# Performance work log

Hardware: AMD Instinct MI355X
Metric: run time of the kernel (lower is better)

## Reference

```python
import jax, jax.numpy as jnp
import numpy as np

D_MODEL = 1024
NUM_HEADS = 16
DEPTH = D_MODEL // NUM_HEADS
B, S = 8, 1024


def setup_inputs() -> dict:
    key = jax.random.key(0)
    ks = jax.random.split(key, 12)
    sc = 0.02
    return {
        "v": jax.random.normal(ks[0], (B, S, D_MODEL), jnp.float32),
        "k": jax.random.normal(ks[1], (B, S, D_MODEL), jnp.float32),
        "q_in": jax.random.normal(ks[2], (B, S, D_MODEL), jnp.float32),
        "mask": jnp.zeros((B, 1, 1, S), jnp.float32),
        "wq_w": jax.random.normal(ks[3], (D_MODEL, D_MODEL), jnp.float32) * sc,
        "wq_b": jnp.zeros((D_MODEL,), jnp.float32),
        "wk_w": jax.random.normal(ks[4], (D_MODEL, D_MODEL), jnp.float32) * sc,
        "wk_b": jnp.zeros((D_MODEL,), jnp.float32),
        "wv_w": jax.random.normal(ks[5], (D_MODEL, D_MODEL), jnp.float32) * sc,
        "wv_b": jnp.zeros((D_MODEL,), jnp.float32),
        "wo_w": jax.random.normal(ks[6], (2 * D_MODEL, D_MODEL), jnp.float32) * sc,
        "wo_b": jnp.zeros((D_MODEL,), jnp.float32),
    }


def _split_heads(x):
    # (B, S, D) -> (B, H, S, depth)
    b, s, _ = x.shape
    return x.reshape(b, s, NUM_HEADS, DEPTH).transpose(0, 2, 1, 3)


def reference(v, k, q_in, mask, wq_w, wq_b, wk_w, wk_b, wv_w, wv_b, wo_w, wo_b):
    q = _split_heads(q_in @ wq_w + wq_b)   # (B,H,Sq,depth)
    kk = _split_heads(k @ wk_w + wk_b)     # (B,H,Sk,depth)
    vv = _split_heads(v @ wv_w + wv_b)     # (B,H,Sk,depth)

    scale = 1.0 / jnp.sqrt(jnp.float32(DEPTH))
    logits = jnp.einsum("bhqd,bhkd->bhqk", q, kk) * scale
    logits = logits + mask * (-1e9)
    attn = jax.nn.softmax(logits, axis=-1)  # dropout inactive (inference)
    ctx = jnp.einsum("bhqk,bhkd->bhqd", attn, vv)

    # (B,H,Sq,depth) -> (B,Sq,D)
    ctx = ctx.transpose(0, 2, 1, 3).reshape(q_in.shape[0], -1, D_MODEL)
    concat = jnp.concatenate([q_in, ctx], axis=-1)  # (B,Sq,2D)
    out = concat @ wo_w + wo_b
    return out
```

## Files before the change

### kernel.cpp

```cpp
#include <hip/hip_runtime.h>

#define NHEADS 16
#define DEPTH  64
#define BATCH  8
#define SEQ    1024
#define DMODEL 1024
#define MTOT   (BATCH*SEQ)

typedef float f32x4 __attribute__((ext_vector_type(4)));
typedef int   i32x4 __attribute__((ext_vector_type(4)));
typedef unsigned short u16;

static __device__ inline u16 f2bf(float x) {
    unsigned int u = __builtin_bit_cast(unsigned int, x);
    u += 0x7FFFu + ((u >> 16) & 1u);
    return (u16)(u >> 16);
}

static __device__ inline unsigned cvt_pk_bf16(float lo, float hi) {
    unsigned r;
    asm("v_cvt_pk_bf16_f32 %0, %1, %2" : "=v"(r) : "v"(lo), "v"(hi));
    return r;
}

static __device__ inline void mfma_bf16(f32x4& acc, i32x4 a, i32x4 b) {
    asm("v_mfma_f32_16x16x32_bf16 %0, %1, %2, %0" : "+v"(acc) : "v"(a), "v"(b));
}

static __device__ inline void gload16(const u16* g, u16* l) {
    __builtin_amdgcn_global_load_lds(
        (const __attribute__((address_space(1))) void*)g,
        (__attribute__((address_space(3))) void*)l,
        16, 0, 0);
}

__global__ __launch_bounds__(256) void cvt_kernel(
    const float* __restrict__ A, const float* __restrict__ B, const float* __restrict__ C,
    u16* __restrict__ Ao, u16* __restrict__ Bo, u16* __restrict__ Co)
{
    const float* src = (blockIdx.y == 0) ? A : (blockIdx.y == 1) ? B : C;
    u16* dst         = (blockIdx.y == 0) ? Ao : (blockIdx.y == 1) ? Bo : Co;
    int i = (blockIdx.x * 256 + threadIdx.x) * 8;
    float4 f0 = *reinterpret_cast<const float4*>(src + i);
    float4 f1 = *reinterpret_cast<const float4*>(src + i + 4);
    uint4 u;
    u.x = cvt_pk_bf16(f0.x, f0.y);
    u.y = cvt_pk_bf16(f0.z, f0.w);
    u.z = cvt_pk_bf16(f1.x, f1.y);
    u.w = cvt_pk_bf16(f1.z, f1.w);
    *reinterpret_cast<uint4*>(dst + i) = u;
}

__global__ __launch_bounds__(256) void transpose_cvt_kernel(
    const float* __restrict__ W, u16* __restrict__ Wt, int K, int N)
{
    __shared__ u16 tile[32][33];
    int n0 = blockIdx.x * 32, k0 = blockIdx.y * 32;
    int tx = threadIdx.x & 31, ty = threadIdx.x >> 5;
    #pragma unroll
    for (int r = 0; r < 32; r += 8)
        tile[r + ty][tx] = f2bf(W[(k0 + r + ty) * N + n0 + tx]);
    __syncthreads();
    #pragma unroll
    for (int r = 0; r < 32; r += 8)
        Wt[(n0 + r + ty) * K + k0 + tx] = tile[tx][r + ty];
}

__global__ __launch_bounds__(256) void proj_kernel(
    const u16* __restrict__ Xq, const u16* __restrict__ Xk, const u16* __restrict__ Xv,
    const u16* __restrict__ Wtq, const u16* __restrict__ Wtk, const u16* __restrict__ Wtv,
    const float* __restrict__ Bq, const float* __restrict__ Bk, const float* __restrict__ Bv,
    u16* __restrict__ Qh, u16* __restrict__ Kh, u16* __restrict__ Vt)
{
    const int z = blockIdx.z;
    const u16* X    = (z == 0) ? Xq  : (z == 1) ? Xk  : Xv;
    const u16* Wt   = (z == 0) ? Wtq : (z == 1) ? Wtk : Wtv;
    const float* Bi = (z == 0) ? Bq  : (z == 1) ? Bk  : Bv;
    u16* Out        = (z == 0) ? Qh  : (z == 1) ? Kh  : Vt;

    __shared__ u16 As[128 * 64];
    __shared__ u16 Bs[128 * 64];

    const int t = threadIdx.x;
    const int m0 = blockIdx.x * 128, n0 = blockIdx.y * 128;
    const int lane = t & 63, w = t >> 6;
    const int wu = __builtin_amdgcn_readfirstlane(w);
    const int wm = w >> 1, wn = w & 1;
    const int lr = lane & 15, lg = lane >> 4;
    const int srow = lane >> 3;
    const int scol = ((lane & 7) ^ (srow & 7)) * 8;

    const u16* ga = X  + (m0 + wu * 32 + srow) * DMODEL + scol;
    const u16* gb = Wt + (n0 + wu * 32 + srow) * DMODEL + scol;
    u16* la = As + wu * 32 * 64;
    u16* lb = Bs + wu * 32 * 64;

    f32x4 acc[4][4];
    #pragma unroll
    for (int i = 0; i < 4; ++i)
        #pragma unroll
        for (int j = 0; j < 4; ++j) acc[i][j] = f32x4{0.f, 0.f, 0.f, 0.f};

    for (int k0 = 0; k0 < DMODEL; k0 += 64) {
        __syncthreads();
        gload16(ga + k0,               la);
        gload16(ga + k0 +  8 * DMODEL, la +  8 * 64);
        gload16(ga + k0 + 16 * DMODEL, la + 16 * 64);
        gload16(ga + k0 + 24 * DMODEL, la + 24 * 64);
        gload16(gb + k0,               lb);
        gload16(gb + k0 +  8 * DMODEL, lb +  8 * 64);
        gload16(gb + k0 + 16 * DMODEL, lb + 16 * 64);
        gload16(gb + k0 + 24 * DMODEL, lb + 24 * 64);
        __syncthreads();
        #pragma unroll
        for (int kk = 0; kk < 2; ++kk) {
            const int pslot = ((kk * 4 + lg) ^ (lr & 7)) << 3;
            i32x4 af[4], bfr[4];
            #pragma unroll
            for (int mi = 0; mi < 4; ++mi)
                af[mi] = *reinterpret_cast<const i32x4*>(
                    &As[(wm * 64 + mi * 16 + lr) * 64 + pslot]);
            #pragma unroll
            for (int ni = 0; ni < 4; ++ni)
                bfr[ni] = *reinterpret_cast<const i32x4*>(
                    &Bs[(wn * 64 + ni * 16 + lr) * 64 + pslot]);
            #pragma unroll
            for (int mi = 0; mi < 4; ++mi)
                #pragma unroll
                for (int ni = 0; ni < 4; ++ni)
                    mfma_bf16(acc[mi][ni], af[mi], bfr[ni]);
        }
    }
    asm volatile("s_nop 7\n\ts_nop 7");
    #pragma unroll
    for (int mi = 0; mi < 4; ++mi)
        #pragma unroll
        for (int ni = 0; ni < 4; ++ni) {
            int n = n0 + wn * 64 + ni * 16 + lr;
            float bv = Bi[n];
            int h = n >> 6, d = n & 63;
            int mb = m0 + wm * 64 + mi * 16 + lg * 4;
            int b = mb >> 10, srw = mb & 1023;
            if (z == 2) {
                uint2 u;
                u.x = cvt_pk_bf16(acc[mi][ni][0] + bv, acc[mi][ni][1] + bv);
                u.y = cvt_pk_bf16(acc[mi][ni][2] + bv, acc[mi][ni][3] + bv);
                *reinterpret_cast<uint2*>(&Vt[(((b << 4) + h) * DEPTH + d) * SEQ + srw]) = u;
            } else if (z == 0) {
                #pragma unroll
                for (int r = 0; r < 4; ++r)
                    Out[(((b << 4) + h) * SEQ + srw + r) * DEPTH + d] = f2bf((acc[mi][ni][r] + bv) * 0.18033688f);
            } else {
                #pragma unroll
                for (int r = 0; r < 4; ++r)
                    Out[(((b << 4) + h) * SEQ + srw + r) * DEPTH + d] = f2bf(acc[mi][ni][r] + bv);
            }
        }
}

__global__ __launch_bounds__(256) void attn_kernel(
    const u16* __restrict__ Qh, const u16* __restrict__ Kh, const u16* __restrict__ Vt,
    const float* __restrict__ mask, u16* __restrict__ CTX)
{
    __shared__ u16 Ks[64 * 64];
    __shared__ u16 Vts[64 * 64];
    __shared__ u16 Ps[4][32 * 64];
    __shared__ float Ms[SEQ];

    const int t = threadIdx.x;
    const int lane = t & 63, w = t >> 6;
    const int lr = lane & 15, lg = lane >> 4;
    const int bh = blockIdx.y;
    const int b = bh >> 4, h = bh & 15;
    const int qw = blockIdx.x * 128 + w * 32;

    const u16* Qp = Qh + bh * (SEQ * DEPTH);
    const u16* Kp = Kh + bh * (SEQ * DEPTH);
    const u16* Vp = Vt + bh * (SEQ * DEPTH);

    {
        float4 mv = *reinterpret_cast<const float4*>(mask + b * SEQ + t * 4);
        const float mk = -1.4426950408889634e9f;
        Ms[t * 4 + 0] = mv.x * mk;
        Ms[t * 4 + 1] = mv.y * mk;
        Ms[t * 4 + 2] = mv.z * mk;
        Ms[t * 4 + 3] = mv.w * mk;
    }

    i32x4 aq[2][2];
    #pragma unroll
    for (int g = 0; g < 2; ++g) {
        aq[g][0] = *reinterpret_cast<const i32x4*>(&Qp[(qw + g * 16 + lr) * DEPTH + lg * 8]);
        aq[g][1] = *reinterpret_cast<const i32x4*>(&Qp[(qw + g * 16 + lr) * DEPTH + 32 + lg * 8]);
    }

    f32x4 ctx[2][4];
    #pragma unroll
    for (int g = 0; g < 2; ++g)
        #pragma unroll
        for (int i = 0; i < 4; ++i) ctx[g][i] = f32x4{0.f, 0.f, 0.f, 0.f};
    float psum[2] = {0.f, 0.f};

    const int r0 = t >> 3;
    const int c8 = t & 7;
    const int swz0 = (c8 ^ (r0 & 7)) * 8;
    u16* kd0 = Ks  + r0 * 64 + swz0;
    u16* kd1 = Ks  + (r0 + 32) * 64 + swz0;
    u16* vd0 = Vts + r0 * 64 + swz0;
    u16* vd1 = Vts + (r0 + 32) * 64 + swz0;
    const u16* ksrc0 = Kp + r0 * DEPTH + c8 * 8;
    const u16* ksrc1 = Kp + (r0 + 32) * DEPTH + c8 * 8;
    const u16* vsrc0 = Vp + r0 * SEQ + c8 * 8;
    const u16* vsrc1 = Vp + (r0 + 32) * SEQ + c8 * 8;
    u16* PsW = Ps[w];

    u16* pdst[2][4];
    #pragma unroll
    for (int g = 0; g < 2; ++g)
        #pragma unroll
        for (int tt = 0; tt < 4; ++tt) {
            int slot = tt * 2 + (lg >> 1);
            pdst[g][tt] = PsW + (g * 16 + lr) * 64 + ((slot ^ (lr & 7)) << 3) + ((lg & 1) << 2);
        }

    uint4 kr0 = *reinterpret_cast<const uint4*>(ksrc0);
    uint4 kr1 = *reinterpret_cast<const uint4*>(ksrc1);
    uint4 vr0 = *reinterpret_cast<const uint4*>(vsrc0);
    uint4 vr1 = *reinterpret_cast<const uint4*>(vsrc1);

    for (int kt = 0; kt < SEQ; kt += 64) {
        __syncthreads();
        *reinterpret_cast<uint4*>(kd0) = kr0;
        *reinterpret_cast<uint4*>(kd1) = kr1;
        *reinterpret_cast<uint4*>(vd0) = vr0;
        *reinterpret_cast<uint4*>(vd1) = vr1;
        if (kt + 64 < SEQ) {
            int kn = kt + 64;
            kr0 = *reinterpret_cast<const uint4*>(ksrc0 + kn * DEPTH);
            kr1 = *reinterpret_cast<const uint4*>(ksrc1 + kn * DEPTH);
            vr0 = *reinterpret_cast<const uint4*>(vsrc0 + kn);
            vr1 = *reinterpret_cast<const uint4*>(vsrc1 + kn);
        }
        __syncthreads();

        f32x4 sc[2][4];
        #pragma unroll
        for (int g = 0; g < 2; ++g)
            #pragma unroll
            for (int i = 0; i < 4; ++i) sc[g][i] = f32x4{0.f, 0.f, 0.f, 0.f};
        #pragma unroll
        for (int tt = 0; tt < 4; ++tt) {
            int row = tt * 16 + lr, rs = row & 7;
            const u16* kr = Ks + row * 64;
            i32x4 bk0 = *reinterpret_cast<const i32x4*>(kr + ((lg ^ rs) << 3));
            i32x4 bk1 = *reinterpret_cast<const i32x4*>(kr + (((4 + lg) ^ rs) << 3));
            mfma_bf16(sc[0][tt], bk0, aq[0][0]);
            mfma_bf16(sc[0][tt], bk1, aq[0][1]);
            mfma_bf16(sc[1][tt], bk0, aq[1][0]);
            mfma_bf16(sc[1][tt], bk1, aq[1][1]);
        }
        asm volatile("s_nop 7\n\ts_nop 7");

        #pragma unroll
        for (int tt = 0; tt < 4; ++tt) {
            float4 m4 = *reinterpret_cast<const float4*>(&Ms[kt + tt * 16 + lg * 4]);
            #pragma unroll
            for (int g = 0; g < 2; ++g) {
                float p0 = __builtin_amdgcn_exp2f(sc[g][tt][0] + m4.x);
                float p1 = __builtin_amdgcn_exp2f(sc[g][tt][1] + m4.y);
                float p2 = __builtin_amdgcn_exp2f(sc[g][tt][2] + m4.z);
                float p3 = __builtin_amdgcn_exp2f(sc[g][tt][3] + m4.w);
                psum[g] += (p0 + p1) + (p2 + p3);
                uint2 u;
                u.x = cvt_pk_bf16(p0, p1);
                u.y = cvt_pk_bf16(p2, p3);
                *reinterpret_cast<uint2*>(pdst[g][tt]) = u;
            }
        }

        const int rswz = lr & 7;
        i32x4 pa[2][2];
        #pragma unroll
        for (int g = 0; g < 2; ++g) {
            const u16* pr = PsW + (g * 16 + lr) * 64;
            pa[g][0] = *reinterpret_cast<const i32x4*>(pr + ((lg ^ rswz) << 3));
            pa[g][1] = *reinterpret_cast<const i32x4*>(pr + (((4 + lg) ^ rswz) << 3));
        }
        #pragma unroll
        for (int dt = 0; dt < 4; ++dt) {
            int dcol = dt * 16 + lr, ds = dcol & 7;
            const u16* vr = Vts + dcol * 64;
            i32x4 bv0 = *reinterpret_cast<const i32x4*>(vr + ((lg ^ ds) << 3));
            i32x4 bv1 = *reinterpret_cast<const i32x4*>(vr + (((4 + lg) ^ ds) << 3));
            mfma_bf16(ctx[0][dt], pa[0][0], bv0);
            mfma_bf16(ctx[0][dt], pa[0][1], bv1);
            mfma_bf16(ctx[1][dt], pa[1][0], bv0);
            mfma_bf16(ctx[1][dt], pa[1][1], bv1);
        }
    }
    asm volatile("s_nop 7\n\ts_nop 7");
    #pragma unroll
    for (int g = 0; g < 2; ++g) {
        psum[g] += __shfl_xor(psum[g], 16);
        psum[g] += __shfl_xor(psum[g], 32);
    }
    float inv0 = 1.f / psum[0];
    float inv1 = 1.f / psum[1];
    #pragma unroll
    for (int g = 0; g < 2; ++g) {
        float invr[4];
        #pragma unroll
        for (int r = 0; r < 4; ++r)
            invr[r] = __shfl(g ? inv1 : inv0, lg * 4 + r);
        #pragma unroll
        for (int dt = 0; dt < 4; ++dt)
            #pragma unroll
            for (int r = 0; r < 4; ++r) {
                int s = qw + g * 16 + lg * 4 + r;
                int d = dt * 16 + lr;
                CTX[(b * SEQ + s) * DMODEL + h * DEPTH + d] = f2bf(ctx[g][dt][r] * invr[r]);
            }
    }
}

__global__ __launch_bounds__(256) void outproj_kernel(
    const float* __restrict__ Xq, const u16* __restrict__ CTX,
    const u16* __restrict__ Wto,
    const float* __restrict__ Bo, float* __restrict__ Out)
{
    __shared__ u16 As[128][40];
    __shared__ u16 Bs[128 * 32];

    const int t = threadIdx.x;
    const int m0 = blockIdx.x * 128, n0 = blockIdx.y * 128;
    const int lane = t & 63, w = t >> 6;
    const int wu = __builtin_amdgcn_readfirstlane(w);
    const int wm = w >> 1, wn = w & 1;
    const int lr = lane & 15, lg = lane >> 4;
    const int srow = t >> 1, scb = (t & 1) * 16;
    const int brow = lane >> 2;
    const int bcol = ((lane & 3) ^ (brow & 3)) * 8;

    const u16* gb = Wto + (n0 + wu * 32 + brow) * (2 * DMODEL) + bcol;
    u16* lb = Bs + wu * 32 * 32;

    f32x4 acc[4][4];
    #pragma unroll
    for (int i = 0; i < 4; ++i)
        #pragma unroll
        for (int j = 0; j < 4; ++j) acc[i][j] = f32x4{0.f, 0.f, 0.f, 0.f};

    for (int k0 = 0; k0 < 2 * DMODEL; k0 += 32) {
        __syncthreads();
        gload16(gb + k0, lb);
        gload16(gb + k0 + 16 * (2 * DMODEL), lb + 16 * 32);
        if (k0 < DMODEL) {
            const float* s = Xq + (m0 + srow) * DMODEL + k0 + scb;
            float4 f0 = *reinterpret_cast<const float4*>(s);
            float4 f1 = *reinterpret_cast<const float4*>(s + 4);
            float4 f2 = *reinterpret_cast<const float4*>(s + 8);
            float4 f3 = *reinterpret_cast<const float4*>(s + 12);
            uint4 u0, u1;
            u0.x = cvt_pk_bf16(f0.x, f0.y);
            u0.y = cvt_pk_bf16(f0.z, f0.w);
            u0.z = cvt_pk_bf16(f1.x, f1.y);
            u0.w = cvt_pk_bf16(f1.z, f1.w);
            u1.x = cvt_pk_bf16(f2.x, f2.y);
            u1.y = cvt_pk_bf16(f2.z, f2.w);
            u1.z = cvt_pk_bf16(f3.x, f3.y);
            u1.w = cvt_pk_bf16(f3.z, f3.w);
            *reinterpret_cast<uint4*>(&As[srow][scb])     = u0;
            *reinterpret_cast<uint4*>(&As[srow][scb + 8]) = u1;
        } else {
            const u16* s = CTX + (m0 + srow) * DMODEL + (k0 - DMODEL) + scb;
            *reinterpret_cast<uint4*>(&As[srow][scb])     = *reinterpret_cast<const uint4*>(s);
            *reinterpret_cast<uint4*>(&As[srow][scb + 8]) = *reinterpret_cast<const uint4*>(s + 8);
        }
        __syncthreads();
        i32x4 af[4], bfr[4];
        #pragma unroll
        for (int mi = 0; mi < 4; ++mi)
            af[mi] = *reinterpret_cast<const i32x4*>(&As[wm * 64 + mi * 16 + lr][lg * 8]);
        #pragma unroll
        for (int ni = 0; ni < 4; ++ni)
            bfr[ni] = *reinterpret_cast<const i32x4*>(
                &Bs[(wn * 64 + ni * 16 + lr) * 32 + ((lg ^ (lr & 3)) << 3)]);
        #pragma unroll
        for (int mi = 0; mi < 4; ++mi)
            #pragma unroll
            for (int ni = 0; ni < 4; ++ni)
                mfma_bf16(acc[mi][ni], af[mi], bfr[ni]);
    }
    asm volatile("s_nop 7\n\ts_nop 7");
    #pragma unroll
    for (int mi = 0; mi < 4; ++mi)
        #pragma unroll
        for (int ni = 0; ni < 4; ++ni) {
            int n = n0 + wn * 64 + ni * 16 + lr;
            float bv = Bo[n];
            #pragma unroll
            for (int r = 0; r < 4; ++r) {
                int m = m0 + wm * 64 + mi * 16 + lg * 4 + r;
                Out[m * DMODEL + n] = acc[mi][ni][r] + bv;
            }
        }
}

extern "C" void kernel_launch(void* const* d_in, const int* in_sizes, int n_in,
                              void* d_out, int out_size, void* d_ws, size_t ws_size,
                              hipStream_t stream) {
    const float* v    = (const float*)d_in[0];
    const float* k    = (const float*)d_in[1];
    const float* q_in = (const float*)d_in[2];
    const float* mask = (const float*)d_in[3];
    const float* wq_w = (const float*)d_in[4];
    const float* wq_b = (const float*)d_in[5];
    const float* wk_w = (const float*)d_in[6];
    const float* wk_b = (const float*)d_in[7];
    const float* wv_w = (const float*)d_in[8];
    const float* wv_b = (const float*)d_in[9];
    const float* wo_w = (const float*)d_in[10];
    const float* wo_b = (const float*)d_in[11];
    float* out = (float*)d_out;

    u16* ws  = (u16*)d_ws;
    u16* Wtq = ws;
    u16* Wtk = Wtq + (1u << 20);
    u16* Wtv = Wtk + (1u << 20);
    u16* Wto = Wtv + (1u << 20);
    u16* Qh  = Wto + (2u << 20);
    u16* Kh  = Qh + (8u << 20);
    u16* Vt  = Kh + (8u << 20);
    u16* CTX = Vt + (8u << 20);

    u16* Xbq = CTX;
    u16* Xbk = (u16*)d_out;
    u16* Xbv = (u16*)d_out + (8u << 20);

    cvt_kernel<<<dim3(4096, 3), 256, 0, stream>>>(q_in, k, v, Xbq, Xbk, Xbv);

    transpose_cvt_kernel<<<dim3(32, 32), 256, 0, stream>>>(wq_w, Wtq, 1024, 1024);
    transpose_cvt_kernel<<<dim3(32, 32), 256, 0, stream>>>(wk_w, Wtk, 1024, 1024);
    transpose_cvt_kernel<<<dim3(32, 32), 256, 0, stream>>>(wv_w, Wtv, 1024, 1024);
    transpose_cvt_kernel<<<dim3(32, 64), 256, 0, stream>>>(wo_w, Wto, 2048, 1024);

    proj_kernel<<<dim3(64, 8, 3), 256, 0, stream>>>(
        Xbq, Xbk, Xbv, Wtq, Wtk, Wtv, wq_b, wk_b, wv_b, Qh, Kh, Vt);

    attn_kernel<<<dim3(8, 128), 256, 0, stream>>>(Qh, Kh, Vt, mask, CTX);

    outproj_kernel<<<dim3(64, 8), 256, 0, stream>>>(q_in, CTX, Wto, wo_b, out);
}
```

Baseline: 198.8 us.

## Double K-tile depth in outproj and load CTX via direct-to-LDS gloads

The output-projection GEMM now advances K by 64 per iteration instead of 32, so each iteration carries twice as much MFMA work and the loop runs half as many barriers. The context half of the A operand is loaded with the direct global-to-LDS gload16 path instead of going through registers. Both LDS tiles use an XOR-swizzled 64-wide layout to avoid bank conflicts. The cost is more shared memory per block, which may lower occupancy.

```diff
diff --git a/kernel.cpp b/kernel.cpp
--- a/kernel.cpp
+++ b/kernel.cpp
@@ -328,8 +328,8 @@
     const u16* __restrict__ Wto,
     const float* __restrict__ Bo, float* __restrict__ Out)
 {
-    __shared__ u16 As[128][40];
-    __shared__ u16 Bs[128 * 32];
+    __shared__ u16 As[128 * 64];
+    __shared__ u16 Bs[128 * 64];
 
     const int t = threadIdx.x;
     const int m0 = blockIdx.x * 128, n0 = blockIdx.y * 128;
@@ -337,12 +337,15 @@
     const int wu = __builtin_amdgcn_readfirstlane(w);
     const int wm = w >> 1, wn = w & 1;
     const int lr = lane & 15, lg = lane >> 4;
-    const int srow = t >> 1, scb = (t & 1) * 16;
-    const int brow = lane >> 2;
-    const int bcol = ((lane & 3) ^ (brow & 3)) * 8;
-
-    const u16* gb = Wto + (n0 + wu * 32 + brow) * (2 * DMODEL) + bcol;
-    u16* lb = Bs + wu * 32 * 32;
+    const int srow = lane >> 3;
+    const int scol = ((lane & 7) ^ (srow & 7)) * 8;
+
+    const int arow = t >> 1, ahalf = t & 1;
+
+    const u16* gac = CTX + (m0 + wu * 32 + srow) * DMODEL + scol;
+    const u16* gb  = Wto + (n0 + wu * 32 + srow) * (2 * DMODEL) + scol;
+    u16* la = As + wu * 32 * 64;
+    u16* lb = Bs + wu * 32 * 64;
 
     f32x4 acc[4][4];
     #pragma unroll
@@ -350,46 +353,52 @@
         #pragma unroll
         for (int j = 0; j < 4; ++j) acc[i][j] = f32x4{0.f, 0.f, 0.f, 0.f};
 
-    for (int k0 = 0; k0 < 2 * DMODEL; k0 += 32) {
-        __syncthreads();
-        gload16(gb + k0, lb);
-        gload16(gb + k0 + 16 * (2 * DMODEL), lb + 16 * 32);
+    for (int k0 = 0; k0 < 2 * DMODEL; k0 += 64) {
+        __syncthreads();
+        gload16(gb + k0,                      lb);
+        gload16(gb + k0 +  8 * 2 * DMODEL,    lb +  8 * 64);
+        gload16(gb + k0 + 16 * 2 * DMODEL,    lb + 16 * 64);
+        gload16(gb + k0 + 24 * 2 * DMODEL,    lb + 24 * 64);
         if (k0 < DMODEL) {
-            const float* s = Xq + (m0 + srow) * DMODEL + k0 + scb;
-            float4 f0 = *reinterpret_cast<const float4*>(s);
-            float4 f1 = *reinterpret_cast<const float4*>(s + 4);
-            float4 f2 = *reinterpret_cast<const float4*>(s + 8);
-            float4 f3 = *reinterpret_cast<const float4*>(s + 12);
-            uint4 u0, u1;
-            u0.x = cvt_pk_bf16(f0.x, f0.y);
-            u0.y = cvt_pk_bf16(f0.z, f0.w);
-            u0.z = cvt_pk_bf16(f1.x, f1.y);
-            u0.w = cvt_pk_bf16(f1.z, f1.w);
-            u1.x = cvt_pk_bf16(f2.x, f2.y);
-            u1.y = cvt_pk_bf16(f2.z, f2.w);
-            u1.z = cvt_pk_bf16(f3.x, f3.y);
-            u1.w = cvt_pk_bf16(f3.z, f3.w);
-            *reinterpret_cast<uint4*>(&As[srow][scb])     = u0;
-            *reinterpret_cast<uint4*>(&As[srow][scb + 8]) = u1;
+            const float* s = Xq + (m0 + arow) * DMODEL + k0 + ahalf * 32;
+            #pragma unroll
+            for (int j = 0; j < 4; ++j) {
+                float4 fa = *reinterpret_cast<const float4*>(s + j * 8);
+                float4 fb = *reinterpret_cast<const float4*>(s + j * 8 + 4);
+                uint4 u;
+                u.x = cvt_pk_bf16(fa.x, fa.y);
+                u.y = cvt_pk_bf16(fa.z, fa.w);
+                u.z = cvt_pk_bf16(fb.x, fb.y);
+                u.w = cvt_pk_bf16(fb.z, fb.w);
+                int slot = ahalf * 4 + j;
+                *reinterpret_cast<uint4*>(&As[arow * 64 + ((slot ^ (arow & 7)) << 3)]) = u;
+            }
         } else {
-            const u16* s = CTX + (m0 + srow) * DMODEL + (k0 - DMODEL) + scb;
-            *reinterpret_cast<uint4*>(&As[srow][scb])     = *reinterpret_cast<const uint4*>(s);
-            *reinterpret_cast<uint4*>(&As[srow][scb + 8]) = *reinterpret_cast<const uint4*>(s + 8);
-        }
-        __syncthreads();
-        i32x4 af[4], bfr[4];
-        #pragma unroll
-        for (int mi = 0; mi < 4; ++mi)
-            af[mi] = *reinterpret_cast<const i32x4*>(&As[wm * 64 + mi * 16 + lr][lg * 8]);
-        #pragma unroll
-        for (int ni = 0; ni < 4; ++ni)
-            bfr[ni] = *reinterpret_cast<const i32x4*>(
-                &Bs[(wn * 64 + ni * 16 + lr) * 32 + ((lg ^ (lr & 3)) << 3)]);
-        #pragma unroll
-        for (int mi = 0; mi < 4; ++mi)
+            int kc = k0 - DMODEL;
+            gload16(gac + kc,               la);
+            gload16(gac + kc +  8 * DMODEL, la +  8 * 64);
+            gload16(gac + kc + 16 * DMODEL, la + 16 * 64);
+            gload16(gac + kc + 24 * DMODEL, la + 24 * 64);
+        }
+        __syncthreads();
+        #pragma unroll
+        for (int kk = 0; kk < 2; ++kk) {
+            const int pslot = ((kk * 4 + lg) ^ (lr & 7)) << 3;
+            i32x4 af[4], bfr[4];
+            #pragma unroll
+            for (int mi = 0; mi < 4; ++mi)
+                af[mi] = *reinterpret_cast<const i32x4*>(
+                    &As[(wm * 64 + mi * 16 + lr) * 64 + pslot]);
             #pragma unroll
             for (int ni = 0; ni < 4; ++ni)
-                mfma_bf16(acc[mi][ni], af[mi], bfr[ni]);
+                bfr[ni] = *reinterpret_cast<const i32x4*>(
+                    &Bs[(wn * 64 + ni * 16 + lr) * 64 + pslot]);
+            #pragma unroll
+            for (int mi = 0; mi < 4; ++mi)
+                #pragma unroll
+                for (int ni = 0; ni < 4; ++ni)
+                    mfma_bf16(acc[mi][ni], af[mi], bfr[ni]);
+        }
     }
     asm volatile("s_nop 7\n\ts_nop 7");
     #pragma unroll
```

New measurement: 204.5 us. 2.9% more time.
